# Performance work log

Hardware: AMD Instinct MI355X
Metric: run time of the kernel (lower is better)

## Reference

```python
import jax, jax.numpy as jnp
import numpy as np

IH, IW = 32, 32
HEADS, DIM_HEAD = 8, 32
EPS = 1e-6


def conv3x3(x, w):
    # x: [B,C,H,W], w: [O,I,3,3], stride 1, pad 1, no bias
    return jax.lax.conv_general_dilated(x, w, (1, 1), ((1, 1), (1, 1)),
                                        dimension_numbers=('NCHW', 'OIHW', 'NCHW'))


def groupnorm1(x, g, b):
    # GroupNorm(1, C): normalize over (C,H,W) per sample
    mu = jnp.mean(x, axis=(1, 2, 3), keepdims=True)
    var = jnp.var(x, axis=(1, 2, 3), keepdims=True)
    xn = (x - mu) * jax.lax.rsqrt(var + EPS)
    return xn * g[None, :, None, None] + b[None, :, None, None]


def proj(x, w, g, b):
    return jax.nn.gelu(groupnorm1(conv3x3(x, w), g, b), approximate=False)


def relative_index(ih, iw):
    coords = np.stack(np.meshgrid(np.arange(ih), np.arange(iw), indexing='ij')).reshape(2, -1)
    rel = coords[:, :, None] - coords[:, None, :]  # [2, n, n]
    rel[0] += ih - 1
    rel[1] += iw - 1
    rel[0] *= 2 * iw - 1
    return jnp.asarray(rel.sum(0).reshape(-1))  # [n*n]


def setup_inputs() -> dict:
    key = jax.random.key(0)
    ks = jax.random.split(key, 9)
    C = HEADS * DIM_HEAD  # 256
    B = 8
    s = 0.02
    inp = {
        'x': jax.random.normal(ks[0], (B, C, IH, IW), jnp.float32),
        'wq': jax.random.normal(ks[1], (C, C, 3, 3), jnp.float32) * s,
        'wk': jax.random.normal(ks[2], (C, C, 3, 3), jnp.float32) * s,
        'wv': jax.random.normal(ks[3], (C, C, 3, 3), jnp.float32) * s,
        'gq': jnp.ones((C,), jnp.float32), 'bq': jnp.zeros((C,), jnp.float32),
        'gk': jnp.ones((C,), jnp.float32), 'bk': jnp.zeros((C,), jnp.float32),
        'gv': jnp.ones((C,), jnp.float32), 'bv': jnp.zeros((C,), jnp.float32),
        'bias_table': jax.random.normal(ks[4], ((2 * IH - 1) * (2 * IW - 1), HEADS), jnp.float32) * s,
        'wo': jax.random.normal(ks[5], (C, C), jnp.float32) * s,
        'bo': jnp.zeros((C,), jnp.float32),
    }
    return inp


def reference(x, wq, wk, wv, gq, bq, gk, bk, gv, bv, bias_table, wo, bo):
    B, C, ih, iw = x.shape
    n = ih * iw
    h, d = HEADS, DIM_HEAD

    q = proj(x, wq, gq, bq)  # [B,C,H,W]
    k = proj(x, wk, gk, bk)
    v = proj(x, wv, gv, bv)

    # 'b c ih iw -> b (ih iw) c' then 'b n (h d) -> b h n d'  ==  [B,h,d,n] -> [B,h,n,d]
    def to_heads(t):
        return t.reshape(B, h, d, n).transpose(0, 1, 3, 2)

    q4, k4, v4 = to_heads(q), to_heads(k), to_heads(v)

    # NOTE: original code applies self.scale only when y is not None; y=None here -> no scale.
    dots = jnp.einsum('bhnd,bhmd->bhnm', q4, k4)  # [B,h,n,n]

    rel_idx = relative_index(ih, iw)  # [n*n]
    rel_bias = bias_table[rel_idx].reshape(n, n, h).transpose(2, 0, 1)[None]  # [1,h,n,n]

    attn = jax.nn.softmax(dots + rel_bias, axis=-1)
    out = jnp.einsum('bhnm,bhmd->bhnd', attn, v4)  # [B,h,n,d]

    # 'b h n d -> b n (h d)' then 'b (ih iw) c -> b c ih iw'
    out = out.transpose(0, 2, 1, 3).reshape(B, n, C).transpose(0, 2, 1).reshape(B, C, ih, iw)

    # to_out: 1x1 conv with bias (dropout=0 in eval)
    out = jnp.einsum('oc,bchw->bohw', wo, out) + bo[None, :, None, None]
    return out
```

## Files before the change

### kernel.cpp

```cpp
#include <hip/hip_runtime.h>
#include <cstdint>
#include <cstddef>

#define GEPS 1e-6f

using bf16x8 = __attribute__((ext_vector_type(8))) short;
using f32x4  = __attribute__((ext_vector_type(4))) float;

__device__ inline ushort f2bf(float x) {
    union { float f; uint32_t u; } v; v.f = x;
    uint32_t r = (v.u + 0x7fffu + ((v.u >> 16) & 1u)) >> 16;
    return (ushort)r;
}
__device__ inline float bf2f(ushort b) {
    union { float f; uint32_t u; } v; v.u = ((uint32_t)b) << 16;
    return v.f;
}

__device__ inline void gll16(const void* g, void* l) {
    __builtin_amdgcn_global_load_lds(
        (const __attribute__((address_space(1))) void*)g,
        (__attribute__((address_space(3))) void*)l, 16, 0, 0);
}

__global__ __launch_bounds__(256) void pack_k(
    const float* __restrict__ wq, const float* __restrict__ wk,
    const float* __restrict__ wv, const float* __restrict__ wo,
    ushort* __restrict__ Wbuf, ushort* __restrict__ wo_bf)
{
    int blk = blockIdx.x, tid = threadIdx.x;
    if (blk < 768) {
        __shared__ ushort Ws[2304];
        int proj = blk >> 8, co = blk & 255;
        const float* src = ((proj == 0) ? wq : ((proj == 1) ? wk : wv)) + (size_t)co * 2304;
#pragma unroll
        for (int j = 0; j < 9; ++j) {
            int idx = j * 256 + tid;
            Ws[idx] = f2bf(src[idx]);
        }
        __syncthreads();
        ushort* dst = Wbuf + (size_t)blk * 2304;
#pragma unroll
        for (int j = 0; j < 9; ++j)
            dst[j * 256 + tid] = Ws[tid * 9 + j];
        return;
    }
    int t = (blk - 768) * 256 + tid;
    float4 v = *(const float4*)&wo[(size_t)t * 4];
    union { uint2 u; ushort s[4]; } o;
    o.s[0] = f2bf(v.x); o.s[1] = f2bf(v.y); o.s[2] = f2bf(v.z); o.s[3] = f2bf(v.w);
    *(uint2*)&wo_bf[(size_t)t * 4] = o.u;
}

__global__ __launch_bounds__(256) void bx_k(const float* __restrict__ btab,
                                            ushort* __restrict__ Bx)
{
    int g = blockIdx.x * 4 + (threadIdx.x >> 6);
    int l = threadIdx.x & 63;
    int h = g >> 10, qt = (g >> 4) & 63, kt = g & 15;
    int quad = l >> 4, c = l & 15;
    union { uint4 v[2]; ushort s[16]; } o;
#pragma unroll
    for (int f = 0; f < 4; ++f)
#pragma unroll
        for (int r = 0; r < 4; ++r) {
            int qrow = qt * 16 + quad * 4 + r;
            int key = kt * 64 + f * 16 + c;
            int dy = (qrow >> 5) - (key >> 5) + 31;
            int dx = (qrow & 31) - (key & 31) + 31;
            o.s[f * 4 + r] = f2bf(btab[(dy * 63 + dx) * 8 + h]);
        }
    uint4* dst = (uint4*)(Bx + ((size_t)g * 64 + l) * 16);
    dst[0] = o.v[0];
    dst[1] = o.v[1];
}

__global__ __launch_bounds__(256) void im2col_k(const float* __restrict__ x,
                                                ushort* __restrict__ Ab)
{
    __shared__ __align__(16) ushort Xs[3 * 34 * 128];
    int tid = threadIdx.x;
    int blk = blockIdx.x;
    int b = blk >> 6, py = (blk >> 1) & 31, half = blk & 1;

#pragma unroll
    for (int p = tid; p < 768; p += 256) {
        int yy = p >> 8;
        int q = p & 255;
        int col = (q >> 7) ? 33 : 0;
        int ci = q & 127;
        Xs[(yy * 34 + col) * 128 + ci] = 0;
    }

#pragma unroll
    for (int it = 0; it < 12; ++it) {
        int j = it * 256 + tid;
        int ci_l = j / 24;
        int o = (j - ci_l * 24) * 4;
        int yy = o >> 5, xx = o & 31;
        int row = py - 1 + yy;
        float4 v = make_float4(0.f, 0.f, 0.f, 0.f);
        if (row >= 0 && row < 32)
            v = *(const float4*)&x[((size_t)(b * 256 + half * 128 + ci_l)) * 1024 + row * 32 + xx];
        int base = (yy * 34 + xx + 1) * 128 + ci_l;
        Xs[base + 0 * 128] = f2bf(v.x);
        Xs[base + 1 * 128] = f2bf(v.y);
        Xs[base + 2 * 128] = f2bf(v.z);
        Xs[base + 3 * 128] = f2bf(v.w);
    }
    __syncthreads();

    ushort* dst = Ab + (size_t)(b * 1024 + py * 32) * 2304;
#pragma unroll
    for (int it = 0; it < 18; ++it) {
        int idx = it * 256 + tid;
        int ci8l = idx & 15;
        int tp = (idx >> 4) % 9;
        int px = idx / 144;
        int kh = tp / 3, kw = tp - kh * 3;
        uint4 p = *(const uint4*)&Xs[(kh * 34 + px + kw) * 128 + ci8l * 8];
        *(uint4*)&dst[(size_t)(px * 288 + tp * 32 + half * 16 + ci8l) * 8] = p;
    }
}

__global__ __launch_bounds__(256, 3) void gemm_bt(
    const ushort* __restrict__ A, const ushort* __restrict__ B,
    int M, int N, int K,
    float* __restrict__ Cpart,
    float* __restrict__ Cout, const float* __restrict__ bias, int mode)
{
    __shared__ __align__(16) ushort As[128 * 64];
    __shared__ __align__(16) ushort Bs[128 * 64];
    int tid = threadIdx.x;
    int mbase = blockIdx.x * 128, nbase = blockIdx.y * 128;
    int kspan = K / gridDim.z;
    int k0 = blockIdx.z * kspan;
    int wave = tid >> 6, lane = tid & 63;
    int wm = wave & 1, wn = wave >> 1;
    int quad = lane >> 4, c = lane & 15;

    int row_s = tid >> 3;
    int cc8 = (tid & 7) ^ (row_s & 7);
    ushort* ldsA = As + wave * 512;
    ushort* ldsB = Bs + wave * 512;

    f32x4 acc[4][4];
#pragma unroll
    for (int i = 0; i < 4; ++i)
#pragma unroll
        for (int j = 0; j < 4; ++j) acc[i][j] = (f32x4){0.f, 0.f, 0.f, 0.f};

    for (int kb = k0; kb < k0 + kspan; kb += 64) {
        __syncthreads();
#pragma unroll
        for (int R = 0; R < 4; ++R) {
            int row = R * 32 + row_s;
            gll16(A + (size_t)(mbase + row) * K + kb + cc8 * 8,
                  ldsA + R * 2048);
            gll16(B + (size_t)(nbase + row) * K + kb + cc8 * 8,
                  ldsB + R * 2048);
        }
        __syncthreads();
#pragma unroll
        for (int kq = 0; kq < 2; ++kq) {
            bf16x8 af[4], bfr[4];
            int sw = ((kq * 4 + quad) ^ (c & 7)) * 8;
#pragma unroll
            for (int i = 0; i < 4; ++i) {
                af[i]  = *(const bf16x8*)&As[(wm * 64 + i * 16 + c) * 64 + sw];
                bfr[i] = *(const bf16x8*)&Bs[(wn * 64 + i * 16 + c) * 64 + sw];
            }
#pragma unroll
            for (int i = 0; i < 4; ++i)
#pragma unroll
                for (int j = 0; j < 4; ++j)
                    acc[i][j] = __builtin_amdgcn_mfma_f32_16x16x32_bf16(
                        af[i], bfr[j], acc[i][j], 0, 0, 0);
        }
    }

    if (mode == 0) {
        float* Cp = Cpart + (size_t)blockIdx.z * M * N;
#pragma unroll
        for (int i = 0; i < 4; ++i) {
            int mrow = mbase + wm * 64 + i * 16 + quad * 4;
#pragma unroll
            for (int j = 0; j < 4; ++j) {
                int ncol = nbase + wn * 64 + j * 16 + c;
#pragma unroll
                for (int r = 0; r < 4; ++r)
                    Cp[(size_t)(mrow + r) * N + ncol] = acc[i][j][r];
            }
        }
    } else {
#pragma unroll
        for (int i = 0; i < 4; ++i) {
            int mrow0 = mbase + wm * 64 + i * 16 + quad * 4;
#pragma unroll
            for (int j = 0; j < 4; ++j) {
                int ncol = nbase + wn * 64 + j * 16 + c;
                int bb = ncol >> 10, px = ncol & 1023;
#pragma unroll
                for (int r = 0; r < 4; ++r) {
                    int o = mrow0 + r;
                    Cout[((size_t)bb * 256 + o) * 1024 + px] = acc[i][j][r] + bias[o];
                }
            }
        }
    }
}

__global__ __launch_bounds__(256) void stats1_k(const float* __restrict__ P0,
                                                const float* __restrict__ P1,
                                                float2* __restrict__ part)
{
    int t = blockIdx.x * 256 + threadIdx.x;
    size_t base = (size_t)t * 8;
    float4 a0 = *(const float4*)&P0[base];
    float4 a1 = *(const float4*)&P0[base + 4];
    float4 c0 = *(const float4*)&P1[base];
    float4 c1 = *(const float4*)&P1[base + 4];
    float v[8] = {a0.x + c0.x, a0.y + c0.y, a0.z + c0.z, a0.w + c0.w,
                  a1.x + c1.x, a1.y + c1.y, a1.z + c1.z, a1.w + c1.w};
    float s1 = 0.f, s2 = 0.f;
#pragma unroll
    for (int e = 0; e < 8; ++e) { s1 += v[e]; s2 += v[e] * v[e]; }
#pragma unroll
    for (int mk = 1; mk < 32; mk <<= 1) {
        s1 += __shfl_xor(s1, mk, 64);
        s2 += __shfl_xor(s2, mk, 64);
    }
    if ((threadIdx.x & 31) == 0) {
        int gg = t >> 5;
        int m = gg / 3;
        int proj = gg - m * 3;
        int b = m >> 10, slot = m & 1023;
        part[(proj * 8 + b) * 1024 + slot] = make_float2(s1, s2);
    }
}

__global__ __launch_bounds__(256) void stats2_k(const float2* __restrict__ part,
                                                float* __restrict__ stats)
{
    __shared__ float w1[4], w2[4];
    int s = blockIdx.x, tid = threadIdx.x;
    float s1 = 0.f, s2 = 0.f;
#pragma unroll
    for (int i = 0; i < 4; ++i) {
        float2 v = part[(size_t)s * 1024 + tid * 4 + i];
        s1 += v.x; s2 += v.y;
    }
#pragma unroll
    for (int mk = 1; mk < 64; mk <<= 1) {
        s1 += __shfl_xor(s1, mk, 64);
        s2 += __shfl_xor(s2, mk, 64);
    }
    if ((tid & 63) == 0) { w1[tid >> 6] = s1; w2[tid >> 6] = s2; }
    __syncthreads();
    if (tid == 0) {
        stats[s * 2 + 0] = w1[0] + w1[1] + w1[2] + w1[3];
        stats[s * 2 + 1] = w2[0] + w2[1] + w2[2] + w2[3];
    }
}

__global__ void gn_k(const float* __restrict__ P0, const float* __restrict__ P1,
                     const float* __restrict__ stats,
                     const float* __restrict__ gq, const float* __restrict__ bq,
                     const float* __restrict__ gk, const float* __restrict__ bk,
                     const float* __restrict__ gv, const float* __restrict__ bv,
                     ushort* __restrict__ qb, ushort* __restrict__ kb2,
                     ushort* __restrict__ vx)
{
    int t = blockIdx.x * 256 + threadIdx.x;
    int m = t / 96;
    int nn = (t - m * 96) * 8;
    int proj = nn >> 8, co = nn & 255;
    int b = m >> 10, px = m & 1023;
    float s1 = stats[(proj * 8 + b) * 2 + 0];
    float s2 = stats[(proj * 8 + b) * 2 + 1];
    const float Ninv = 1.f / 262144.f;
    float mu = s1 * Ninv;
    float var = fmaxf(s2 * Ninv - mu * mu, 0.f);
    float rsig = rsqrtf(var + GEPS);
    const float* gam = (proj == 0) ? gq : ((proj == 1) ? gk : gv);
    const float* bet = (proj == 0) ? bq : ((proj == 1) ? bk : bv);

    size_t base = (size_t)m * 768 + nn;
    float4 a0 = *(const float4*)&P0[base];
    float4 a1 = *(const float4*)&P0[base + 4];
    float4 c0 = *(const float4*)&P1[base];
    float4 c1 = *(const float4*)&P1[base + 4];
    float xv[8] = {a0.x + c0.x, a0.y + c0.y, a0.z + c0.z, a0.w + c0.w,
                   a1.x + c1.x, a1.y + c1.y, a1.z + c1.z, a1.w + c1.w};
    union { uint4 v; ushort s[8]; } outp;
#pragma unroll
    for (int e = 0; e < 8; ++e) {
        int cc = co + e;
        float xn = (xv[e] - mu) * rsig * gam[cc] + bet[cc];
        float ge = 0.5f * xn * (1.f + erff(xn * 0.70710678118654752f));
        outp.s[e] = f2bf(ge);
    }
    int h = co >> 5, d = co & 31;
    if (proj == 0) {
        *(uint4*)(qb + ((((size_t)b * 8 + h) * 1024 + px) * 32 + d)) = outp.v;
    } else if (proj == 1) {
        *(uint4*)(kb2 + ((((size_t)b * 8 + h) * 1024 + px) * 32 + d)) = outp.v;
    } else {
        ushort* vb = vx + ((size_t)b * 8 + h) * 32768;
        int kca = px >> 5, quad = (px >> 3) & 3, j = px & 7;
#pragma unroll
        for (int e = 0; e < 8; ++e) {
            int dd = d + e;
            vb[(((kca * 2 + (dd >> 4)) * 64) + quad * 16 + (dd & 15)) * 8 + j] = outp.s[e];
        }
    }
}

__global__ __launch_bounds__(256, 2) void attn_k(
    const ushort* __restrict__ qb, const ushort* __restrict__ kb,
    const ushort* __restrict__ vx, const ushort* __restrict__ Bx,
    ushort* __restrict__ attnout)
{
    __shared__ __align__(16) ushort Pl[4 * 16 * 72];
    int tid = threadIdx.x, wave = tid >> 6, lane = tid & 63;
    int quad = lane >> 4, c = lane & 15;
    int bh = blockIdx.y;
    int h = bh & 7, b = bh >> 3;
    int qbase = blockIdx.x * 64 + wave * 16;

    const ushort* Q  = qb + (size_t)bh * 1024 * 32;
    const ushort* Kp = kb + (size_t)bh * 1024 * 32;
    const ushort* Vb = vx + (size_t)bh * 32768;
    const ushort* bxp = Bx + (((size_t)(h * 64 + (qbase >> 4)) * 16) * 64 + lane) * 16;
    ushort* Pw = Pl + wave * 16 * 72;

    bf16x8 qf = *(const bf16x8*)&Q[(qbase + c) * 32 + quad * 8];

    float l_[4] = {0.f, 0.f, 0.f, 0.f};
    f32x4 Of0 = {0.f, 0.f, 0.f, 0.f}, Of1 = {0.f, 0.f, 0.f, 0.f};

    for (int kb64 = 0; kb64 < 1024; kb64 += 64) {
        f32x4 S[4];
        f32x4 zf = {0.f, 0.f, 0.f, 0.f};
#pragma unroll
        for (int f = 0; f < 4; ++f) {
            bf16x8 kf = *(const bf16x8*)&Kp[(kb64 + f * 16 + c) * 32 + quad * 8];
            S[f] = __builtin_amdgcn_mfma_f32_16x16x32_bf16(qf, kf, zf, 0, 0, 0);
        }
        union { uint4 v[2]; ushort s[16]; } bu;
        const uint4* bsrc = (const uint4*)(bxp + (size_t)(kb64 >> 6) * 1024);
        bu.v[0] = bsrc[0];
        bu.v[1] = bsrc[1];
#pragma unroll
        for (int f = 0; f < 4; ++f)
#pragma unroll
            for (int r = 0; r < 4; ++r) {
                float p = __expf(S[f][r] + bf2f(bu.s[f * 4 + r]));
                S[f][r] = p;
                l_[r] += p;
            }
#pragma unroll
        for (int f = 0; f < 4; ++f)
#pragma unroll
            for (int r = 0; r < 4; ++r)
                Pw[(quad * 4 + r) * 72 + f * 16 + c] = f2bf(S[f][r]);
#pragma unroll
        for (int kc = 0; kc < 2; ++kc) {
            int kca = (kb64 >> 5) + kc;
            bf16x8 pf = *(const bf16x8*)&Pw[c * 72 + kc * 32 + quad * 8];
            bf16x8 vf0 = *(const bf16x8*)&Vb[((kca * 2 + 0) * 64 + lane) * 8];
            Of0 = __builtin_amdgcn_mfma_f32_16x16x32_bf16(pf, vf0, Of0, 0, 0, 0);
            bf16x8 vf1 = *(const bf16x8*)&Vb[((kca * 2 + 1) * 64 + lane) * 8];
            Of1 = __builtin_amdgcn_mfma_f32_16x16x32_bf16(pf, vf1, Of1, 0, 0, 0);
        }
    }
#pragma unroll
    for (int r = 0; r < 4; ++r) {
        float l = l_[r];
        l += __shfl_xor(l, 1, 64);
        l += __shfl_xor(l, 2, 64);
        l += __shfl_xor(l, 4, 64);
        l += __shfl_xor(l, 8, 64);
        float inv = 1.f / l;
        int qr = qbase + quad * 4 + r;
        size_t base = ((size_t)b * 1024 + qr) * 256 + h * 32;
        attnout[base + c]      = f2bf(Of0[r] * inv);
        attnout[base + 16 + c] = f2bf(Of1[r] * inv);
    }
}

extern "C" void kernel_launch(void* const* d_in, const int* in_sizes, int n_in,
                              void* d_out, int out_size, void* d_ws, size_t ws_size,
                              hipStream_t stream)
{
    const float* x    = (const float*)d_in[0];
    const float* wq   = (const float*)d_in[1];
    const float* wk   = (const float*)d_in[2];
    const float* wv   = (const float*)d_in[3];
    const float* gq   = (const float*)d_in[4];
    const float* bq   = (const float*)d_in[5];
    const float* gk   = (const float*)d_in[6];
    const float* bk   = (const float*)d_in[7];
    const float* gv   = (const float*)d_in[8];
    const float* bv   = (const float*)d_in[9];
    const float* btab = (const float*)d_in[10];
    const float* wo   = (const float*)d_in[11];
    const float* bo   = (const float*)d_in[12];
    float* out = (float*)d_out;

    char* w = (char*)d_ws;
    size_t off = 0;
    auto alloc = [&](size_t bytes) -> char* {
        char* p = w + off;
        off += (bytes + 255) & ~(size_t)255;
        return p;
    };
    ushort* Abuf    = (ushort*)alloc(8192ull * 2304 * 2);
    ushort* Wbuf    = (ushort*)alloc(768ull * 2304 * 2);
    ushort* wo_bf   = (ushort*)alloc(65536ull * 2);
    float*  P0      = (float*)alloc(8192ull * 768 * 4);
    float*  P1      = (float*)alloc(8192ull * 768 * 4);
    float2* part    = (float2*)alloc(48ull * 1024 * 8);
    float*  stats   = (float*)alloc(384);
    ushort* qb      = (ushort*)Abuf;
    ushort* kb2     = qb  + 8ull * 8 * 1024 * 32;
    ushort* vx      = kb2 + 8ull * 8 * 1024 * 32;
    ushort* attnout = vx  + 8ull * 8 * 32 * 1024;
    ushort* Bx      = attnout + 8192ull * 256;

    pack_k<<<832, 256, 0, stream>>>(wq, wk, wv, wo, Wbuf, wo_bf);
    im2col_k<<<512, 256, 0, stream>>>(x, Abuf);
    gemm_bt<<<dim3(64, 6, 2), 256, 0, stream>>>(Abuf, Wbuf, 8192, 768, 2304,
                                                P0, nullptr, nullptr, 0);
    bx_k<<<2048, 256, 0, stream>>>(btab, Bx);
    stats1_k<<<3072, 256, 0, stream>>>(P0, P1, part);
    stats2_k<<<48, 256, 0, stream>>>(part, stats);
    gn_k<<<3072, 256, 0, stream>>>(P0, P1, stats, gq, bq, gk, bk, gv, bv,
                                   qb, kb2, vx);
    attn_k<<<dim3(16, 64), 256, 0, stream>>>(qb, kb2, vx, Bx, attnout);
    gemm_bt<<<dim3(2, 64, 1), 256, 0, stream>>>(wo_bf, attnout, 256, 8192, 256,
                                                nullptr, out, bo, 1);
}
```

Before: 236.2 us.

## Split attention over key halves with combine pass; merge prep kernels

Merges the weight packing, im2col, wo conversion and bias-table expansion into one prep kernel, which removes two launches. Attention is split across two key halves via a z grid dimension, raising block count and occupancy (launch bounds 8). Each half writes unnormalized fp32 partial outputs and row sums, and a new combine kernel adds them, normalizes and writes bf16. This relies on the softmax exponent having no max subtraction, so the partials add directly, at the cost of extra fp32 traffic and one more launch. Bx moves to its own workspace allocation, since Abuf-aliased memory would be overwritten.

```diff
diff --git a/kernel.cpp b/kernel.cpp
--- a/kernel.cpp
+++ b/kernel.cpp
@@ -23,40 +23,84 @@
         (__attribute__((address_space(3))) void*)l, 16, 0, 0);
 }
 
-__global__ __launch_bounds__(256) void pack_k(
+__global__ __launch_bounds__(256) void prep_k(
+    const float* __restrict__ x,
     const float* __restrict__ wq, const float* __restrict__ wk,
     const float* __restrict__ wv, const float* __restrict__ wo,
-    ushort* __restrict__ Wbuf, ushort* __restrict__ wo_bf)
-{
-    int blk = blockIdx.x, tid = threadIdx.x;
-    if (blk < 768) {
-        __shared__ ushort Ws[2304];
-        int proj = blk >> 8, co = blk & 255;
+    const float* __restrict__ btab,
+    ushort* __restrict__ Ab, ushort* __restrict__ Wbuf,
+    ushort* __restrict__ wo_bf, ushort* __restrict__ Bx)
+{
+    __shared__ __align__(16) ushort Xs[3 * 34 * 128];
+    int tid = threadIdx.x;
+    int blk = blockIdx.x;
+
+    if (blk < 512) {
+        int b = blk >> 6, py = (blk >> 1) & 31, half = blk & 1;
+#pragma unroll
+        for (int p = tid; p < 768; p += 256) {
+            int yy = p >> 8;
+            int q = p & 255;
+            int col = (q >> 7) ? 33 : 0;
+            int ci = q & 127;
+            Xs[(yy * 34 + col) * 128 + ci] = 0;
+        }
+#pragma unroll
+        for (int it = 0; it < 12; ++it) {
+            int j = it * 256 + tid;
+            int ci_l = j / 24;
+            int o = (j - ci_l * 24) * 4;
+            int yy = o >> 5, xx = o & 31;
+            int row = py - 1 + yy;
+            float4 v = make_float4(0.f, 0.f, 0.f, 0.f);
+            if (row >= 0 && row < 32)
+                v = *(const float4*)&x[((size_t)(b * 256 + half * 128 + ci_l)) * 1024 + row * 32 + xx];
+            int base = (yy * 34 + xx + 1) * 128 + ci_l;
+            Xs[base + 0 * 128] = f2bf(v.x);
+            Xs[base + 1 * 128] = f2bf(v.y);
+            Xs[base + 2 * 128] = f2bf(v.z);
+            Xs[base + 3 * 128] = f2bf(v.w);
+        }
+        __syncthreads();
+        ushort* dst = Ab + (size_t)(b * 1024 + py * 32) * 2304;
+#pragma unroll
+        for (int it = 0; it < 18; ++it) {
+            int idx = it * 256 + tid;
+            int ci8l = idx & 15;
+            int tp = (idx >> 4) % 9;
+            int px = idx / 144;
+            int kh = tp / 3, kw = tp - kh * 3;
+            uint4 p = *(const uint4*)&Xs[(kh * 34 + px + kw) * 128 + ci8l * 8];
+            *(uint4*)&dst[(size_t)(px * 288 + tp * 32 + half * 16 + ci8l) * 8] = p;
+        }
+        return;
+    }
+    if (blk < 1280) {
+        int wrow = blk - 512;
+        int proj = wrow >> 8, co = wrow & 255;
         const float* src = ((proj == 0) ? wq : ((proj == 1) ? wk : wv)) + (size_t)co * 2304;
 #pragma unroll
         for (int j = 0; j < 9; ++j) {
             int idx = j * 256 + tid;
-            Ws[idx] = f2bf(src[idx]);
+            Xs[idx] = f2bf(src[idx]);
         }
         __syncthreads();
-        ushort* dst = Wbuf + (size_t)blk * 2304;
+        ushort* dst = Wbuf + (size_t)wrow * 2304;
 #pragma unroll
         for (int j = 0; j < 9; ++j)
-            dst[j * 256 + tid] = Ws[tid * 9 + j];
+            dst[j * 256 + tid] = Xs[tid * 9 + j];
         return;
     }
-    int t = (blk - 768) * 256 + tid;
-    float4 v = *(const float4*)&wo[(size_t)t * 4];
-    union { uint2 u; ushort s[4]; } o;
-    o.s[0] = f2bf(v.x); o.s[1] = f2bf(v.y); o.s[2] = f2bf(v.z); o.s[3] = f2bf(v.w);
-    *(uint2*)&wo_bf[(size_t)t * 4] = o.u;
-}
-
-__global__ __launch_bounds__(256) void bx_k(const float* __restrict__ btab,
-                                            ushort* __restrict__ Bx)
-{
-    int g = blockIdx.x * 4 + (threadIdx.x >> 6);
-    int l = threadIdx.x & 63;
+    if (blk < 1344) {
+        int t = (blk - 1280) * 256 + tid;
+        float4 v = *(const float4*)&wo[(size_t)t * 4];
+        union { uint2 u; ushort s[4]; } o;
+        o.s[0] = f2bf(v.x); o.s[1] = f2bf(v.y); o.s[2] = f2bf(v.z); o.s[3] = f2bf(v.w);
+        *(uint2*)&wo_bf[(size_t)t * 4] = o.u;
+        return;
+    }
+    int g = (blk - 1344) * 4 + (tid >> 6);
+    int l = tid & 63;
     int h = g >> 10, qt = (g >> 4) & 63, kt = g & 15;
     int quad = l >> 4, c = l & 15;
     union { uint4 v[2]; ushort s[16]; } o;
@@ -73,54 +117,6 @@
     uint4* dst = (uint4*)(Bx + ((size_t)g * 64 + l) * 16);
     dst[0] = o.v[0];
     dst[1] = o.v[1];
-}
-
-__global__ __launch_bounds__(256) void im2col_k(const float* __restrict__ x,
-                                                ushort* __restrict__ Ab)
-{
-    __shared__ __align__(16) ushort Xs[3 * 34 * 128];
-    int tid = threadIdx.x;
-    int blk = blockIdx.x;
-    int b = blk >> 6, py = (blk >> 1) & 31, half = blk & 1;
-
-#pragma unroll
-    for (int p = tid; p < 768; p += 256) {
-        int yy = p >> 8;
-        int q = p & 255;
-        int col = (q >> 7) ? 33 : 0;
-        int ci = q & 127;
-        Xs[(yy * 34 + col) * 128 + ci] = 0;
-    }
-
-#pragma unroll
-    for (int it = 0; it < 12; ++it) {
-        int j = it * 256 + tid;
-        int ci_l = j / 24;
-        int o = (j - ci_l * 24) * 4;
-        int yy = o >> 5, xx = o & 31;
-        int row = py - 1 + yy;
-        float4 v = make_float4(0.f, 0.f, 0.f, 0.f);
-        if (row >= 0 && row < 32)
-            v = *(const float4*)&x[((size_t)(b * 256 + half * 128 + ci_l)) * 1024 + row * 32 + xx];
-        int base = (yy * 34 + xx + 1) * 128 + ci_l;
-        Xs[base + 0 * 128] = f2bf(v.x);
-        Xs[base + 1 * 128] = f2bf(v.y);
-        Xs[base + 2 * 128] = f2bf(v.z);
-        Xs[base + 3 * 128] = f2bf(v.w);
-    }
-    __syncthreads();
-
-    ushort* dst = Ab + (size_t)(b * 1024 + py * 32) * 2304;
-#pragma unroll
-    for (int it = 0; it < 18; ++it) {
-        int idx = it * 256 + tid;
-        int ci8l = idx & 15;
-        int tp = (idx >> 4) % 9;
-        int px = idx / 144;
-        int kh = tp / 3, kw = tp - kh * 3;
-        uint4 p = *(const uint4*)&Xs[(kh * 34 + px + kw) * 128 + ci8l * 8];
-        *(uint4*)&dst[(size_t)(px * 288 + tp * 32 + half * 16 + ci8l) * 8] = p;
-    }
 }
 
 __global__ __launch_bounds__(256, 3) void gemm_bt(
@@ -316,16 +312,17 @@
     }
 }
 
-__global__ __launch_bounds__(256, 2) void attn_k(
+__global__ __launch_bounds__(256, 8) void attn_k(
     const ushort* __restrict__ qb, const ushort* __restrict__ kb,
     const ushort* __restrict__ vx, const ushort* __restrict__ Bx,
-    ushort* __restrict__ attnout)
+    float* __restrict__ Opart, float* __restrict__ lpart)
 {
     __shared__ __align__(16) ushort Pl[4 * 16 * 72];
     int tid = threadIdx.x, wave = tid >> 6, lane = tid & 63;
     int quad = lane >> 4, c = lane & 15;
     int bh = blockIdx.y;
-    int h = bh & 7, b = bh >> 3;
+    int h = bh & 7;
+    int z = blockIdx.z;
     int qbase = blockIdx.x * 64 + wave * 16;
 
     const ushort* Q  = qb + (size_t)bh * 1024 * 32;
@@ -339,7 +336,7 @@
     float l_[4] = {0.f, 0.f, 0.f, 0.f};
     f32x4 Of0 = {0.f, 0.f, 0.f, 0.f}, Of1 = {0.f, 0.f, 0.f, 0.f};
 
-    for (int kb64 = 0; kb64 < 1024; kb64 += 64) {
+    for (int kb64 = z * 512; kb64 < z * 512 + 512; kb64 += 64) {
         f32x4 S[4];
         f32x4 zf = {0.f, 0.f, 0.f, 0.f};
 #pragma unroll
@@ -381,12 +378,37 @@
         l += __shfl_xor(l, 2, 64);
         l += __shfl_xor(l, 4, 64);
         l += __shfl_xor(l, 8, 64);
-        float inv = 1.f / l;
         int qr = qbase + quad * 4 + r;
-        size_t base = ((size_t)b * 1024 + qr) * 256 + h * 32;
-        attnout[base + c]      = f2bf(Of0[r] * inv);
-        attnout[base + 16 + c] = f2bf(Of1[r] * inv);
-    }
+        size_t ob = (((size_t)z * 64 + bh) * 1024 + qr) * 32;
+        Opart[ob + c]      = Of0[r];
+        Opart[ob + 16 + c] = Of1[r];
+        if (c == 0) lpart[(size_t)z * 65536 + bh * 1024 + qr] = l;
+    }
+}
+
+__global__ __launch_bounds__(256) void combine_k(const float* __restrict__ Opart,
+                                                 const float* __restrict__ lpart,
+                                                 ushort* __restrict__ attnout)
+{
+    int t = blockIdx.x * 256 + threadIdx.x;
+    int g = t & 3;
+    int qg = t >> 2;
+    int bh = qg >> 10, qr = qg & 1023;
+    int b = bh >> 3, h = bh & 7;
+    size_t ob = ((size_t)qg) * 32 + g * 8;
+    float4 o00 = *(const float4*)&Opart[ob];
+    float4 o01 = *(const float4*)&Opart[ob + 4];
+    float4 o10 = *(const float4*)&Opart[(size_t)64 * 1024 * 32 + ob];
+    float4 o11 = *(const float4*)&Opart[(size_t)64 * 1024 * 32 + ob + 4];
+    float inv = 1.f / (lpart[qg] + lpart[65536 + qg]);
+    float v[8] = {(o00.x + o10.x) * inv, (o00.y + o10.y) * inv,
+                  (o00.z + o10.z) * inv, (o00.w + o10.w) * inv,
+                  (o01.x + o11.x) * inv, (o01.y + o11.y) * inv,
+                  (o01.z + o11.z) * inv, (o01.w + o11.w) * inv};
+    union { uint4 u; ushort s[8]; } o;
+#pragma unroll
+    for (int e = 0; e < 8; ++e) o.s[e] = f2bf(v[e]);
+    *(uint4*)&attnout[(((size_t)b * 1024 + qr) * 256) + h * 32 + g * 8] = o.u;
 }
 
 extern "C" void kernel_launch(void* const* d_in, const int* in_sizes, int n_in,
@@ -418,26 +440,28 @@
     ushort* Abuf    = (ushort*)alloc(8192ull * 2304 * 2);
     ushort* Wbuf    = (ushort*)alloc(768ull * 2304 * 2);
     ushort* wo_bf   = (ushort*)alloc(65536ull * 2);
+    ushort* Bx      = (ushort*)alloc(8192ull * 64 * 16 * 2);
     float*  P0      = (float*)alloc(8192ull * 768 * 4);
     float*  P1      = (float*)alloc(8192ull * 768 * 4);
     float2* part    = (float2*)alloc(48ull * 1024 * 8);
     float*  stats   = (float*)alloc(384);
+    float*  Opart   = (float*)alloc(2ull * 64 * 1024 * 32 * 4);
+    float*  lpart   = (float*)alloc(2ull * 64 * 1024 * 4);
     ushort* qb      = (ushort*)Abuf;
     ushort* kb2     = qb  + 8ull * 8 * 1024 * 32;
     ushort* vx      = kb2 + 8ull * 8 * 1024 * 32;
     ushort* attnout = vx  + 8ull * 8 * 32 * 1024;
-    ushort* Bx      = attnout + 8192ull * 256;
-
-    pack_k<<<832, 256, 0, stream>>>(wq, wk, wv, wo, Wbuf, wo_bf);
-    im2col_k<<<512, 256, 0, stream>>>(x, Abuf);
+
+    prep_k<<<3392, 256, 0, stream>>>(x, wq, wk, wv, wo, btab,
+                                     Abuf, Wbuf, wo_bf, Bx);
     gemm_bt<<<dim3(64, 6, 2), 256, 0, stream>>>(Abuf, Wbuf, 8192, 768, 2304,
                                                 P0, nullptr, nullptr, 0);
-    bx_k<<<2048, 256, 0, stream>>>(btab, Bx);
     stats1_k<<<3072, 256, 0, stream>>>(P0, P1, part);
     stats2_k<<<48, 256, 0, stream>>>(part, stats);
     gn_k<<<3072, 256, 0, stream>>>(P0, P1, stats, gq, bq, gk, bk, gv, bv,
                                    qb, kb2, vx);
-    attn_k<<<dim3(16, 64), 256, 0, stream>>>(qb, kb2, vx, Bx, attnout);
+    attn_k<<<dim3(16, 64, 2), 256, 0, stream>>>(qb, kb2, vx, Bx, Opart, lpart);
+    combine_k<<<1024, 256, 0, stream>>>(Opart, lpart, attnout);
     gemm_bt<<<dim3(2, 64, 1), 256, 0, stream>>>(wo_bf, attnout, 256, 8192, 256,
                                                 nullptr, out, bo, 1);
 }
```

Measured after the change: 231.2 us. 1.02x faster.
